# Kernel optimization log

Measured on AMD Instinct MI355X. Metric: run time of the kernel, lower is better.

## Reference

```python
import jax, jax.numpy as jnp
import numpy as np

N = 50000
E = 640000
H = 128
C = 3

def _xavier(key, shape, gain=1.0):
    fan_in, fan_out = shape[0], shape[1]
    a = gain * np.sqrt(6.0 / (fan_in + fan_out))
    return jax.random.uniform(key, shape, jnp.float32, -a, a)

def setup_inputs() -> dict:
    key = jax.random.key(0)
    ks = jax.random.split(key, 12)
    h = jax.random.normal(ks[0], (N, H), jnp.float32)
    x = jax.random.normal(ks[1], (N, C), jnp.float32)
    edge_index = jax.random.randint(ks[2], (2, E), 0, N, jnp.int64 if jax.config.jax_enable_x64 else jnp.int32)
    # edge_mlp: Linear(2H+1 -> H), SiLU, Linear(H -> H), SiLU
    We1 = _xavier(ks[3], (2 * H + 1, H)); be1 = jnp.zeros((H,), jnp.float32)
    We2 = _xavier(ks[4], (H, H));          be2 = jnp.zeros((H,), jnp.float32)
    # coord_mlp: Linear(H -> H), SiLU, Linear(H -> 1, no bias, gain 0.01)
    Wc1 = _xavier(ks[5], (H, H)); bc1 = jnp.zeros((H,), jnp.float32)
    Wc2 = _xavier(ks[6], (H, 1), gain=0.01)
    # node_mlp: Linear(2H -> H), SiLU, Linear(H -> H)
    Wn1 = _xavier(ks[7], (2 * H, H)); bn1 = jnp.zeros((H,), jnp.float32)
    Wn2 = _xavier(ks[8], (H, H));     bn2 = jnp.zeros((H,), jnp.float32)
    return dict(h=h, x=x, edge_index=edge_index,
                We1=We1, be1=be1, We2=We2, be2=be2,
                Wc1=Wc1, bc1=bc1, Wc2=Wc2,
                Wn1=Wn1, bn1=bn1, Wn2=Wn2, bn2=bn2)

def reference(h, x, edge_index, We1, be1, We2, be2, Wc1, bc1, Wc2, Wn1, bn1, Wn2, bn2):
    src, dst = edge_index[0], edge_index[1]
    n = h.shape[0]
    rel_pos = x[src] - x[dst]                              # [E, C]
    dist_sq = jnp.sum(rel_pos * rel_pos, axis=-1, keepdims=True)  # [E, 1]
    edge_input = jnp.concatenate([h[src], h[dst], dist_sq], axis=-1)  # [E, 2H+1]
    m_ij = jax.nn.silu(edge_input @ We1 + be1)
    m_ij = jax.nn.silu(m_ij @ We2 + be2)                   # [E, H]
    coord_weight = jax.nn.silu(m_ij @ Wc1 + bc1) @ Wc2     # [E, 1]
    coord_agg = jax.ops.segment_sum(rel_pos * coord_weight, dst, num_segments=n)
    x_out = x + coord_agg
    msg_agg = jax.ops.segment_sum(m_ij, dst, num_segments=n)  # [N, H]
    node_input = jnp.concatenate([h, msg_agg], axis=-1)    # [N, 2H]
    h_upd = jax.nn.silu(node_input @ Wn1 + bn1) @ Wn2 + bn2
    h_out = h + h_upd
    return (h_out, x_out)
```

## Files before the change

kernel.cpp:

```cpp
#include <hip/hip_runtime.h>

#define H 128

typedef __bf16 bf8_t __attribute__((ext_vector_type(8)));
typedef __bf16 bf2_t __attribute__((ext_vector_type(2)));
typedef float  f4_t  __attribute__((ext_vector_type(4)));

#define MFMA16(a, b, c) __builtin_amdgcn_mfma_f32_16x16x32_bf16((a), (b), (c), 0, 0, 0)

__device__ __forceinline__ float silu_f(float v) {
    return v * (1.0f / (1.0f + __expf(-v)));
}

__device__ __forceinline__ void bar_lds() {
    asm volatile("s_waitcnt lgkmcnt(0)\ns_barrier" ::: "memory");
}

__device__ __forceinline__ float wload(const void* p, int idx, bool f32) {
    return f32 ? ((const float*)p)[idx] : (float)((const __bf16*)p)[idx];
}

__device__ __forceinline__ bf8_t hload8(const void* p, size_t off, bool f32) {
    bf8_t v;
    if (f32) {
        const float4* q = (const float4*)((const float*)p + off);
        const float4 a = q[0], b = q[1];
        v[0]=(__bf16)a.x; v[1]=(__bf16)a.y; v[2]=(__bf16)a.z; v[3]=(__bf16)a.w;
        v[4]=(__bf16)b.x; v[5]=(__bf16)b.y; v[6]=(__bf16)b.z; v[7]=(__bf16)b.w;
    } else {
        v = *(const bf8_t*)((const __bf16*)p + off);
    }
    return v;
}

__device__ __forceinline__ int eidx(const void* ei, int i, bool i64) {
    return i64 ? (int)((const long long*)ei)[i] : ((const int*)ei)[i];
}

__global__ void detect_kernel(const unsigned short* __restrict__ hraw,
                              const int* __restrict__ eiraw, int* __restrict__ flags)
{
    __shared__ int s_nf, s_oddnz;
    if (threadIdx.x == 0) { s_nf = 0; s_oddnz = 0; }
    __syncthreads();
    int nf = 0;
    for (int i = threadIdx.x; i < 16384; i += blockDim.x) {
        const unsigned short u = hraw[i];
        if (((u >> 7) & 0xFF) == 0xFF) nf++;
    }
    int onz = 0;
    for (int i = threadIdx.x; i < 512; i += blockDim.x) {
        if (eiraw[2*i + 1] != 0) onz++;
    }
    if (nf)  atomicAdd(&s_nf, nf);
    if (onz) atomicAdd(&s_oddnz, onz);
    __syncthreads();
    if (threadIdx.x == 0) {
        flags[0] = (s_nf > 0) ? 1 : 0;
        flags[1] = (s_oddnz == 0) ? 1 : 0;
    }
}

__global__ void histd_kernel(const void* __restrict__ ei, int* __restrict__ cnt,
                             const int* __restrict__ flags, int Ee)
{
    const int e = blockIdx.x*blockDim.x + threadIdx.x;
    if (e < Ee) atomicAdd(&cnt[eidx(ei, Ee + e, flags[1] != 0)], 1);
}

__global__ void scanA_kernel(const int* __restrict__ cnt, int* __restrict__ bsum, int Nn)
{
    __shared__ int s[512];
    const int gi = blockIdx.x*512 + threadIdx.x;
    s[threadIdx.x] = (gi < Nn) ? cnt[gi] : 0;
    __syncthreads();
    for (int off = 256; off > 0; off >>= 1) {
        if (threadIdx.x < off) s[threadIdx.x] += s[threadIdx.x + off];
        __syncthreads();
    }
    if (threadIdx.x == 0) bsum[blockIdx.x] = s[0];
}

__global__ void scanB_kernel(int* __restrict__ bsum, int* __restrict__ base, int nCh)
{
    if (threadIdx.x == 0) {
        int acc = 0;
        for (int b = 0; b < nCh; ++b) { base[b] = acc; acc += bsum[b]; }
    }
}

__global__ void scanC_kernel(const int* __restrict__ cnt, const int* __restrict__ base,
                             int* __restrict__ off, int* __restrict__ cursor, int Nn)
{
    __shared__ int s[512];
    const int i  = threadIdx.x;
    const int gi = blockIdx.x*512 + i;
    const int v  = (gi < Nn) ? cnt[gi] : 0;
    s[i] = v;
    __syncthreads();
    for (int o = 1; o < 512; o <<= 1) {
        const int t = (i >= o) ? s[i - o] : 0;
        __syncthreads();
        s[i] += t;
        __syncthreads();
    }
    const int excl = s[i] - v;
    if (gi <= Nn) {
        const int val = base[blockIdx.x] + excl;
        off[gi] = val;
        if (gi < Nn) cursor[gi] = val;
    }
}

__global__ void scatgeo_kernel(const void* __restrict__ ei, int* __restrict__ cursor,
                               int* __restrict__ srcs, int* __restrict__ dsts,
                               float4* __restrict__ rel4, const void* __restrict__ x,
                               const int* __restrict__ flags, int Ee)
{
    const int e = blockIdx.x*blockDim.x + threadIdx.x;
    if (e >= Ee) return;
    const bool i64 = flags[1] != 0;
    const bool f32 = flags[0] != 0;
    const int s = eidx(ei, e, i64);
    const int d = eidx(ei, Ee + e, i64);
    const int p = atomicAdd(&cursor[d], 1);
    srcs[p] = s;
    dsts[p] = d;
    float r[3];
    #pragma unroll
    for (int c = 0; c < 3; ++c)
        r[c] = wload(x, s*3 + c, f32) - wload(x, d*3 + c, f32);
    float4 o; o.x = r[0]; o.y = r[1]; o.z = r[2];
    o.w = r[0]*r[0] + r[1]*r[1] + r[2]*r[2];
    rel4[p] = o;
}

__global__ __launch_bounds__(512, 2)
void proj_kernel(const void* __restrict__ h, const void* __restrict__ We1,
                 const void* __restrict__ be1, const int* __restrict__ flags,
                 __bf16* __restrict__ PB, int Nn)
{
    const bool f32 = flags[0] != 0;
    const int tid  = threadIdx.x;
    const int wv   = tid >> 6;
    const int lane = tid & 63;
    const int quad = lane >> 4;
    const int l15  = lane & 15;

    bf8_t bW[4][2];
    float bias[2];
    #pragma unroll
    for (int t = 0; t < 2; ++t) {
        const int n    = wv*32 + t*16 + l15;
        const int rb   = (n < 128) ? 0 : 128;
        const int col  = n & 127;
        #pragma unroll
        for (int kc = 0; kc < 4; ++kc) {
            bf8_t v;
            #pragma unroll
            for (int j = 0; j < 8; ++j)
                v[j] = (__bf16)wload(We1, (rb + kc*32 + quad*8 + j)*H + col, f32);
            bW[kc][t] = v;
        }
        bias[t] = (n < 128) ? 0.f : wload(be1, col, f32);
    }

    __shared__ __bf16 s_h[32*136];

    const int tiles = (Nn + 31) >> 5;
    for (int tile = blockIdx.x; tile < tiles; tile += gridDim.x) {
        const int nb = tile << 5;
        __syncthreads();
        {
            const int m = tid >> 4, c = tid & 15;
            int node = nb + m; if (node >= Nn) node = Nn - 1;
            *(bf8_t*)&s_h[m*136 + c*8] = hload8(h, (size_t)node*H + c*8, f32);
        }
        __syncthreads();

        f4_t acc[2][2];
        #pragma unroll
        for (int mm = 0; mm < 2; ++mm)
            #pragma unroll
            for (int t = 0; t < 2; ++t) acc[mm][t] = (f4_t){0.f,0.f,0.f,0.f};
        #pragma unroll
        for (int kc = 0; kc < 4; ++kc) {
            #pragma unroll
            for (int mm = 0; mm < 2; ++mm) {
                const bf8_t a = *(const bf8_t*)&s_h[(mm*16 + l15)*136 + quad*8 + kc*32];
                acc[mm][0] = MFMA16(a, bW[kc][0], acc[mm][0]);
                acc[mm][1] = MFMA16(a, bW[kc][1], acc[mm][1]);
            }
        }
        #pragma unroll
        for (int mm = 0; mm < 2; ++mm)
            #pragma unroll
            for (int i = 0; i < 4; ++i) {
                const int row = nb + mm*16 + quad*4 + i;
                if (row < Nn) {
                    #pragma unroll
                    for (int t = 0; t < 2; ++t)
                        PB[(size_t)row*256 + wv*32 + t*16 + l15] =
                            (__bf16)(acc[mm][t][i] + bias[t]);
                }
            }
    }
}

__global__ __launch_bounds__(512, 2)
void egnn_edge_pipe_kernel(const __bf16* __restrict__ PB,
                           const int* __restrict__ srcs, const int* __restrict__ dsts,
                           const float4* __restrict__ rel4,
                           const void* __restrict__ We1,
                           const void* __restrict__ We2, const void* __restrict__ be2,
                           const void* __restrict__ Wc1, const void* __restrict__ bc1,
                           const void* __restrict__ Wc2, const int* __restrict__ flags,
                           float* __restrict__ msg, float* __restrict__ coord,
                           int Ee)
{
    const bool f32 = flags[0] != 0;
    const int tid  = threadIdx.x;
    const int wv   = tid >> 6;
    const int lane = tid & 63;
    const int quad = lane >> 4;
    const int l15  = lane & 15;
    const int mg   = wv >> 2;
    const int ng   = wv & 3;

    bf8_t bW2[4][2], bWc[4][2];
    float be2v[2], bc1v[2], wc2v[2];
    #pragma unroll
    for (int t = 0; t < 2; ++t) {
        const int n = ng*32 + t*16 + l15;
        #pragma unroll
        for (int kc = 0; kc < 4; ++kc) {
            bf8_t v, u;
            #pragma unroll
            for (int j = 0; j < 8; ++j) {
                v[j] = (__bf16)wload(We2, (kc*32 + quad*8 + j)*H + n, f32);
                u[j] = (__bf16)wload(Wc1, (kc*32 + quad*8 + j)*H + n, f32);
            }
            bW2[kc][t] = v;
            bWc[kc][t] = u;
        }
        be2v[t] = wload(be2, n, f32);
        bc1v[t] = wload(bc1, n, f32);
        wc2v[t] = wload(Wc2, n, f32);
    }

    const int em = tid >> 3;
    const int ch = tid & 7;
    float w1dA[8], w1dB[8];
    #pragma unroll
    for (int j = 0; j < 8; ++j) {
        w1dA[j] = wload(We1, 256*H + ch*8 + j, f32);
        w1dB[j] = wload(We1, 256*H + (ch+8)*8 + j, f32);
    }

    __shared__ __bf16 s_m1[64*136];
    __shared__ __bf16 s_m2[64*136];
    __shared__ float  s_cw[4*64];
    __shared__ int    s_dst[2][64];
    __shared__ float4 s_rl[2][64];
    __shared__ float  s_pre[8][128];
    __shared__ float  s_suf[8][128];
    __shared__ int    s_wh[8];

    const int tiles = (Ee + 63) >> 6;
    const float* rw = (const float*)rel4;

    bf8_t rA0, rA1, rB0, rB1;
    float d2cur, d2nxt;
    int   s_n, d_n, d_c;
    float4 r4c, r4n;
    {
        int e0 = blockIdx.x*64 + em; if (e0 >= Ee) e0 = Ee - 1;
        const int sc = srcs[e0], dc = dsts[e0];
        d_c = dc;
        d2cur = rw[(size_t)e0*4 + 3];
        if (ch == 0) r4c = rel4[e0];
        rA0 = *(const bf8_t*)(PB + (size_t)sc*256 + ch*8);
        rA1 = *(const bf8_t*)(PB + (size_t)sc*256 + (ch+8)*8);
        rB0 = *(const bf8_t*)(PB + (size_t)dc*256 + 128 + ch*8);
        rB1 = *(const bf8_t*)(PB + (size_t)dc*256 + 128 + (ch+8)*8);
        const int t1 = blockIdx.x + gridDim.x;
        const int tt = (t1 < tiles) ? t1 : blockIdx.x;
        int e1 = tt*64 + em; if (e1 >= Ee) e1 = Ee - 1;
        s_n = srcs[e1]; d_n = dsts[e1]; d2nxt = rw[(size_t)e1*4 + 3];
        if (ch == 0) r4n = rel4[e1];
    }

    int li = 0;
    for (int t = blockIdx.x; t < tiles; t += gridDim.x, ++li) {
        const int sb = li & 1;
        {
            bf8_t o0, o1;
            #pragma unroll
            for (int j = 0; j < 8; ++j) {
                const float f0 = (float)rA0[j] + (float)rB0[j] + d2cur*w1dA[j];
                const float f1 = (float)rA1[j] + (float)rB1[j] + d2cur*w1dB[j];
                o0[j] = (__bf16)silu_f(f0);
                o1[j] = (__bf16)silu_f(f1);
            }
            *(bf8_t*)&s_m1[em*136 + ch*8]       = o0;
            *(bf8_t*)&s_m1[em*136 + (ch+8)*8]   = o1;
            if (ch == 0) { s_dst[sb][em] = d_c; s_rl[sb][em] = r4c; }
        }
        {
            const int sc = s_n, dc2 = d_n;
            rA0 = *(const bf8_t*)(PB + (size_t)sc*256 + ch*8);
            rA1 = *(const bf8_t*)(PB + (size_t)sc*256 + (ch+8)*8);
            rB0 = *(const bf8_t*)(PB + (size_t)dc2*256 + 128 + ch*8);
            rB1 = *(const bf8_t*)(PB + (size_t)dc2*256 + 128 + (ch+8)*8);
            d_c = d_n; d2cur = d2nxt;
            if (ch == 0) r4c = r4n;
            const int t2 = t + 2*gridDim.x;
            const int tt = (t2 < tiles) ? t2 : t;
            int e2 = tt*64 + em; if (e2 >= Ee) e2 = Ee - 1;
            s_n = srcs[e2]; d_n = dsts[e2]; d2nxt = rw[(size_t)e2*4 + 3];
            if (ch == 0) r4n = rel4[e2];
        }
        bar_lds();

        {
            f4_t a2[2][2];
            #pragma unroll
            for (int mm = 0; mm < 2; ++mm)
                #pragma unroll
                for (int h2 = 0; h2 < 2; ++h2) a2[mm][h2] = (f4_t){0.f,0.f,0.f,0.f};
            #pragma unroll
            for (int kc = 0; kc < 4; ++kc) {
                #pragma unroll
                for (int mm = 0; mm < 2; ++mm) {
                    const bf8_t a = *(const bf8_t*)&s_m1[(mg*32 + mm*16 + l15)*136 + quad*8 + kc*32];
                    a2[mm][0] = MFMA16(a, bW2[kc][0], a2[mm][0]);
                    a2[mm][1] = MFMA16(a, bW2[kc][1], a2[mm][1]);
                }
            }
            #pragma unroll
            for (int mm = 0; mm < 2; ++mm)
                #pragma unroll
                for (int i = 0; i < 4; ++i) {
                    const int m = mg*32 + mm*16 + quad*4 + i;
                    s_m2[m*136 + ng*32 + l15]      = (__bf16)silu_f(a2[mm][0][i] + be2v[0]);
                    s_m2[m*136 + ng*32 + 16 + l15] = (__bf16)silu_f(a2[mm][1][i] + be2v[1]);
                }
        }
        bar_lds();

        {
            f4_t a3[2][2];
            #pragma unroll
            for (int mm = 0; mm < 2; ++mm)
                #pragma unroll
                for (int h2 = 0; h2 < 2; ++h2) a3[mm][h2] = (f4_t){0.f,0.f,0.f,0.f};
            #pragma unroll
            for (int kc = 0; kc < 4; ++kc) {
                #pragma unroll
                for (int mm = 0; mm < 2; ++mm) {
                    const bf8_t a = *(const bf8_t*)&s_m2[(mg*32 + mm*16 + l15)*136 + quad*8 + kc*32];
                    a3[mm][0] = MFMA16(a, bWc[kc][0], a3[mm][0]);
                    a3[mm][1] = MFMA16(a, bWc[kc][1], a3[mm][1]);
                }
            }
            float p[2][4];
            #pragma unroll
            for (int mm = 0; mm < 2; ++mm)
                #pragma unroll
                for (int i = 0; i < 4; ++i) {
                    const float v0 = silu_f(a3[mm][0][i] + bc1v[0]);
                    const float v1 = silu_f(a3[mm][1][i] + bc1v[1]);
                    p[mm][i] = v0*wc2v[0] + v1*wc2v[1];
                }
            #pragma unroll
            for (int off = 1; off < 16; off <<= 1)
                #pragma unroll
                for (int mm = 0; mm < 2; ++mm)
                    #pragma unroll
                    for (int i = 0; i < 4; ++i) p[mm][i] += __shfl_xor(p[mm][i], off, 64);
            if (l15 == 0) {
                #pragma unroll
                for (int mm = 0; mm < 2; ++mm)
                    #pragma unroll
                    for (int i = 0; i < 4; ++i)
                        s_cw[ng*64 + (mg*32 + mm*16 + quad*4 + i)] = p[mm][i];
            }
        }

        {
            const int rbase = wv << 3;
            const int c0    = lane << 1;
            int   curd = __builtin_amdgcn_readfirstlane(s_dst[sb][rbase]);
            float ax = 0.f, ay = 0.f;
            float px = 0.f, py = 0.f;
            int   predone = 0;
            #pragma unroll
            for (int i = 0; i < 8; ++i) {
                const int d = __builtin_amdgcn_readfirstlane(s_dst[sb][rbase + i]);
                const bf2_t v = *(const bf2_t*)&s_m2[(rbase + i)*136 + c0];
                const float vx = (float)v[0], vy = (float)v[1];
                if (d != curd) {
                    if (!predone) { px = ax; py = ay; predone = 1; }
                    else {
                        float2 st; st.x = ax; st.y = ay;
                        *(float2*)&msg[(size_t)curd*H + c0] = st;
                    }
                    curd = d; ax = vx; ay = vy;
                } else { ax += vx; ay += vy; }
            }
            s_pre[wv][c0]   = px;  s_pre[wv][c0+1] = py;
            s_suf[wv][c0]   = ax;  s_suf[wv][c0+1] = ay;
            if (lane == 0) s_wh[wv] = !predone;
        }
        bar_lds();

        if (tid >= 128 && tid < 256) {
            const int c = tid - 128;
            int   curd2 = __builtin_amdgcn_readfirstlane(s_dst[sb][0]);
            float cur   = 0.f;
            int   first = 1;
            #pragma unroll
            for (int gg = 0; gg < 8; ++gg) {
                const int F  = __builtin_amdgcn_readfirstlane(s_dst[sb][gg*8]);
                const int L  = __builtin_amdgcn_readfirstlane(s_dst[sb][gg*8 + 7]);
                const int wh = __builtin_amdgcn_readfirstlane(s_wh[gg]);
                const float preg = s_pre[gg][c];
                const float sufg = s_suf[gg][c];
                if (F != curd2) {
                    if (first) atomicAdd(&msg[(size_t)curd2*H + c], cur);
                    else       msg[(size_t)curd2*H + c] = cur;
                    first = 0; curd2 = F; cur = 0.f;
                }
                if (wh) {
                    cur += sufg;
                } else {
                    cur += preg;
                    if (first) atomicAdd(&msg[(size_t)curd2*H + c], cur);
                    else       msg[(size_t)curd2*H + c] = cur;
                    first = 0; curd2 = L; cur = sufg;
                }
            }
            atomicAdd(&msg[(size_t)curd2*H + c], cur);
        }

        if (tid < 64) {
            const int e = tid;
            const float cwv = s_cw[e] + s_cw[64 + e] + s_cw[128 + e] + s_cw[192 + e];
            const float4 r = s_rl[sb][e];
            const int d = s_dst[sb][e];
            float vx = r.x*cwv, vy = r.y*cwv, vz = r.z*cwv;
            int   cn = 1;
            #pragma unroll
            for (int k = 1; k < 64; k <<= 1) {
                const int   dk = __shfl_up(d,  k, 64);
                const float xk = __shfl_up(vx, k, 64);
                const float yk = __shfl_up(vy, k, 64);
                const float zk = __shfl_up(vz, k, 64);
                const int   ck = __shfl_up(cn, k, 64);
                if (e >= k && dk == d) { vx += xk; vy += yk; vz += zk; cn += ck; }
            }
            const int dnx = __shfl_down(d, 1, 64);
            const bool runend = (e == 63) || (dnx != d);
            if (runend) {
                const int rs = e - cn + 1;
                if (rs == 0 || e == 63) {
                    atomicAdd(&coord[(size_t)d*3 + 0], vx);
                    atomicAdd(&coord[(size_t)d*3 + 1], vy);
                    atomicAdd(&coord[(size_t)d*3 + 2], vz);
                } else {
                    coord[(size_t)d*3 + 0] = vx;
                    coord[(size_t)d*3 + 1] = vy;
                    coord[(size_t)d*3 + 2] = vz;
                }
            }
        }
    }
}

__global__ __launch_bounds__(512, 2)
void egnn_node_kernel(const void* __restrict__ h, const float* __restrict__ msg,
                      const void* __restrict__ Wn1, const void* __restrict__ bn1,
                      const void* __restrict__ Wn2, const void* __restrict__ bn2,
                      const int* __restrict__ flags, void* __restrict__ h_out,
                      const void* __restrict__ x, const float* __restrict__ coord,
                      size_t obase, int do_x, int Nn)
{
    const bool f32 = flags[0] != 0;
    const int tid  = threadIdx.x;
    const int wv   = tid >> 6;
    const int lane = tid & 63;
    const int quad = lane >> 4;
    const int l15  = lane & 15;
    const int mg   = wv >> 2;
    const int ng   = wv & 3;

    bf8_t bW1[8][2];
    bf8_t bW2[4][2];
    float b1v[2], b2v[2];
    #pragma unroll
    for (int t = 0; t < 2; ++t) {
        const int n = ng*32 + t*16 + l15;
        #pragma unroll
        for (int kc = 0; kc < 8; ++kc) {
            bf8_t v;
            #pragma unroll
            for (int j = 0; j < 8; ++j) v[j] = (__bf16)wload(Wn1, (kc*32 + quad*8 + j)*H + n, f32);
            bW1[kc][t] = v;
        }
        #pragma unroll
        for (int kc = 0; kc < 4; ++kc) {
            bf8_t v;
            #pragma unroll
            for (int j = 0; j < 8; ++j) v[j] = (__bf16)wload(Wn2, (kc*32 + quad*8 + j)*H + n, f32);
            bW2[kc][t] = v;
        }
        b1v[t] = wload(bn1, n, f32);
        b2v[t] = wload(bn2, n, f32);
    }

    __shared__ __bf16 s_in[32*264];
    __shared__ __bf16 s_t1[32*136];

    const int tiles = (Nn + 31) >> 5;
    for (int tile = blockIdx.x; tile < tiles; tile += gridDim.x) {
        const int nb = tile << 5;
        __syncthreads();
        #pragma unroll
        for (int r = 0; r < 2; ++r) {
            const int idx = tid + r*512;
            const int m = idx >> 5, c = idx & 31;
            int node = nb + m;
            if (node >= Nn) node = Nn - 1;
            if (c < 16) {
                *(bf8_t*)&s_in[m*264 + c*8] = hload8(h, (size_t)node*H + c*8, f32);
            } else {
                const float4* mp = (const float4*)(msg + (size_t)node*H + (c - 16)*8);
                const float4 v0 = mp[0], v1 = mp[1];
                __bf16* d = &s_in[m*264 + c*8];
                d[0] = (__bf16)v0.x; d[1] = (__bf16)v0.y; d[2] = (__bf16)v0.z; d[3] = (__bf16)v0.w;
                d[4] = (__bf16)v1.x; d[5] = (__bf16)v1.y; d[6] = (__bf16)v1.z; d[7] = (__bf16)v1.w;
            }
        }
        if (do_x && tid < 96) {
            const int m = tid / 3, c = tid - m*3;
            const int node = nb + m;
            if (node < Nn) {
                const float xv = wload(x, node*3 + c, f32);
                const float o = xv + coord[(size_t)node*3 + c];
                if (f32) ((float*)h_out)[obase + (size_t)node*3 + c] = o;
                else     ((__bf16*)h_out)[obase + (size_t)node*3 + c] = (__bf16)o;
            }
        }
        __syncthreads();

        {
            f4_t a0 = {0.f,0.f,0.f,0.f}, a1 = {0.f,0.f,0.f,0.f};
            const int abase = (mg*16 + l15)*264 + quad*8;
            #pragma unroll
            for (int kc = 0; kc < 8; ++kc) {
                const bf8_t a = *(const bf8_t*)&s_in[abase + kc*32];
                a0 = MFMA16(a, bW1[kc][0], a0);
                a1 = MFMA16(a, bW1[kc][1], a1);
            }
            #pragma unroll
            for (int i = 0; i < 4; ++i) {
                const int m = mg*16 + quad*4 + i;
                s_t1[m*136 + ng*32 + l15]      = (__bf16)silu_f(a0[i] + b1v[0]);
                s_t1[m*136 + ng*32 + 16 + l15] = (__bf16)silu_f(a1[i] + b1v[1]);
            }
        }
        __syncthreads();

        {
            f4_t a0 = {0.f,0.f,0.f,0.f}, a1 = {0.f,0.f,0.f,0.f};
            const int abase = (mg*16 + l15)*136 + quad*8;
            #pragma unroll
            for (int kc = 0; kc < 4; ++kc) {
                const bf8_t a = *(const bf8_t*)&s_t1[abase + kc*32];
                a0 = MFMA16(a, bW2[kc][0], a0);
                a1 = MFMA16(a, bW2[kc][1], a1);
            }
            #pragma unroll
            for (int i = 0; i < 4; ++i) {
                const int node = nb + mg*16 + quad*4 + i;
                if (node < Nn) {
                    const int n0 = ng*32 + l15, n1 = n0 + 16;
                    const size_t i0 = (size_t)node*H + n0, i1 = (size_t)node*H + n1;
                    const float h0 = f32 ? ((const float*)h)[i0] : (float)((const __bf16*)h)[i0];
                    const float h1 = f32 ? ((const float*)h)[i1] : (float)((const __bf16*)h)[i1];
                    const float o0 = a0[i] + b2v[0] + h0;
                    const float o1 = a1[i] + b2v[1] + h1;
                    if (f32) {
                        ((float*)h_out)[i0] = o0;
                        ((float*)h_out)[i1] = o1;
                    } else {
                        ((__bf16*)h_out)[i0] = (__bf16)o0;
                        ((__bf16*)h_out)[i1] = (__bf16)o1;
                    }
                }
            }
        }
    }
}

__global__ void cvt_ei_kernel(const void* __restrict__ src, int* __restrict__ dst,
                              int n, const int* __restrict__ flags)
{
    const int i = blockIdx.x*blockDim.x + threadIdx.x;
    if (i >= n) return;
    dst[i] = flags[1] ? (int)((const long long*)src)[i] : ((const int*)src)[i];
}

__global__ __launch_bounds__(512, 2)
void egnn_edge_kernel(const void* __restrict__ h, const void* __restrict__ x,
                      const int* __restrict__ ei,
                      const void* __restrict__ We1, const void* __restrict__ be1,
                      const void* __restrict__ We2, const void* __restrict__ be2,
                      const void* __restrict__ Wc1, const void* __restrict__ bc1,
                      const void* __restrict__ Wc2, const int* __restrict__ flags,
                      float* __restrict__ msg_agg, float* __restrict__ coord_agg,
                      int Nn, int Ee)
{
    const bool f32 = flags[0] != 0;
    const int tid  = threadIdx.x;
    const int wv   = tid >> 6;
    const int lane = tid & 63;
    const int quad = lane >> 4;
    const int l15  = lane & 15;
    const int mg   = wv >> 2;
    const int ng   = wv & 3;

    bf8_t bW1[8][2];
    bf8_t bW2[4][2];
    bf8_t bWc[4][2];
    float be1v[2], be2v[2], bc1v[2], w1dv[2], wc2v[2];
    #pragma unroll
    for (int t = 0; t < 2; ++t) {
        const int n = ng*32 + t*16 + l15;
        #pragma unroll
        for (int kc = 0; kc < 8; ++kc) {
            bf8_t v;
            #pragma unroll
            for (int j = 0; j < 8; ++j) v[j] = (__bf16)wload(We1, (kc*32 + quad*8 + j)*H + n, f32);
            bW1[kc][t] = v;
        }
        #pragma unroll
        for (int kc = 0; kc < 4; ++kc) {
            bf8_t v, u;
            #pragma unroll
            for (int j = 0; j < 8; ++j) {
                v[j] = (__bf16)wload(We2, (kc*32 + quad*8 + j)*H + n, f32);
                u[j] = (__bf16)wload(Wc1, (kc*32 + quad*8 + j)*H + n, f32);
            }
            bW2[kc][t] = v;
            bWc[kc][t] = u;
        }
        be1v[t] = wload(be1, n, f32);
        be2v[t] = wload(be2, n, f32);
        bc1v[t] = wload(bc1, n, f32);
        w1dv[t] = wload(We1, 256*H + n, f32);
        wc2v[t] = wload(Wc2, n, f32);
    }

    __shared__ __bf16 s_in[32*264];
    __shared__ __bf16 s_m1[32*136];
    __shared__ __bf16 s_m2[32*136];
    __shared__ float  s_rel[32*3];
    __shared__ float  s_dist[32];
    __shared__ int    s_dstv[32];
    __shared__ float  s_cw[32*4];

    const int tiles = Ee >> 5;
    for (int tile = blockIdx.x; tile < tiles; tile += gridDim.x) {
        const int ebase = tile << 5;
        __syncthreads();

        if (tid < 32) {
            const int e  = ebase + tid;
            const int sn = ei[e];
            const int dn = ei[Ee + e];
            s_dstv[tid] = dn;
            float d2 = 0.f;
            #pragma unroll
            for (int c = 0; c < 3; ++c) {
                float r;
                if (f32) r = ((const float*)x)[sn*3 + c] - ((const float*)x)[dn*3 + c];
                else     r = (float)((const __bf16*)x)[sn*3 + c] - (float)((const __bf16*)x)[dn*3 + c];
                s_rel[tid*3 + c] = r;
                d2 += r*r;
            }
            s_dist[tid] = d2;
        }
        #pragma unroll
        for (int r = 0; r < 2; ++r) {
            const int idx = tid + r*512;
            const int m = idx >> 5, c = idx & 31;
            const int e = ebase + m;
            const int node = (c < 16) ? ei[e] : ei[Ee + e];
            *(bf8_t*)&s_in[m*264 + c*8] = hload8(h, (size_t)node*H + (c & 15)*8, f32);
        }
        __syncthreads();

        {
            f4_t a0 = {0.f,0.f,0.f,0.f}, a1 = {0.f,0.f,0.f,0.f};
            const int abase = (mg*16 + l15)*264 + quad*8;
            #pragma unroll
            for (int kc = 0; kc < 8; ++kc) {
                const bf8_t a = *(const bf8_t*)&s_in[abase + kc*32];
                a0 = MFMA16(a, bW1[kc][0], a0);
                a1 = MFMA16(a, bW1[kc][1], a1);
            }
            #pragma unroll
            for (int i = 0; i < 4; ++i) {
                const int m = mg*16 + quad*4 + i;
                const float d2 = s_dist[m];
                s_m1[m*136 + ng*32 + l15]      = (__bf16)silu_f(a0[i] + d2*w1dv[0] + be1v[0]);
                s_m1[m*136 + ng*32 + 16 + l15] = (__bf16)silu_f(a1[i] + d2*w1dv[1] + be1v[1]);
            }
        }
        __syncthreads();

        {
            f4_t a0 = {0.f,0.f,0.f,0.f}, a1 = {0.f,0.f,0.f,0.f};
            const int abase = (mg*16 + l15)*136 + quad*8;
            #pragma unroll
            for (int kc = 0; kc < 4; ++kc) {
                const bf8_t a = *(const bf8_t*)&s_m1[abase + kc*32];
                a0 = MFMA16(a, bW2[kc][0], a0);
                a1 = MFMA16(a, bW2[kc][1], a1);
            }
            #pragma unroll
            for (int i = 0; i < 4; ++i) {
                const int m = mg*16 + quad*4 + i;
                const float v0 = silu_f(a0[i] + be2v[0]);
                const float v1 = silu_f(a1[i] + be2v[1]);
                s_m2[m*136 + ng*32 + l15]      = (__bf16)v0;
                s_m2[m*136 + ng*32 + 16 + l15] = (__bf16)v1;
                const size_t db = (size_t)s_dstv[m]*H + ng*32 + l15;
                atomicAdd(&msg_agg[db],      v0);
                atomicAdd(&msg_agg[db + 16], v1);
            }
        }
        __syncthreads();

        {
            f4_t a0 = {0.f,0.f,0.f,0.f}, a1 = {0.f,0.f,0.f,0.f};
            const int abase = (mg*16 + l15)*136 + quad*8;
            #pragma unroll
            for (int kc = 0; kc < 4; ++kc) {
                const bf8_t a = *(const bf8_t*)&s_m2[abase + kc*32];
                a0 = MFMA16(a, bWc[kc][0], a0);
                a1 = MFMA16(a, bWc[kc][1], a1);
            }
            float p[4];
            #pragma unroll
            for (int i = 0; i < 4; ++i) {
                const float v0 = silu_f(a0[i] + bc1v[0]);
                const float v1 = silu_f(a1[i] + bc1v[1]);
                p[i] = v0*wc2v[0] + v1*wc2v[1];
            }
            #pragma unroll
            for (int off = 1; off < 16; off <<= 1) {
                #pragma unroll
                for (int i = 0; i < 4; ++i) p[i] += __shfl_xor(p[i], off, 64);
            }
            if (l15 == 0) {
                #pragma unroll
                for (int i = 0; i < 4; ++i)
                    s_cw[(mg*16 + quad*4 + i)*4 + ng] = p[i];
            }
        }
        __syncthreads();

        if (tid < 96) {
            const int m = tid / 3, c = tid - m*3;
            const float cw = s_cw[m*4 + 0] + s_cw[m*4 + 1] + s_cw[m*4 + 2] + s_cw[m*4 + 3];
            atomicAdd(&coord_agg[(size_t)s_dstv[m]*3 + c], s_rel[m*3 + c]*cw);
        }
    }
}

__global__ void egnn_x_kernel(const void* __restrict__ x, const float* __restrict__ coord_agg,
                              const int* __restrict__ flags, void* __restrict__ out,
                              size_t obase, int total)
{
    const bool f32 = flags[0] != 0;
    const int i = blockIdx.x*blockDim.x + threadIdx.x;
    if (i >= total) return;
    const float xv = f32 ? ((const float*)x)[i] : (float)((const __bf16*)x)[i];
    const float o = xv + coord_agg[i];
    if (f32) ((float*)out)[obase + i] = o;
    else     ((__bf16*)out)[obase + i] = (__bf16)o;
}

static inline size_t align256(size_t v) { return (v + 255) & ~(size_t)255; }

extern "C" void kernel_launch(void* const* d_in, const int* in_sizes, int n_in,
                              void* d_out, int out_size, void* d_ws, size_t ws_size,
                              hipStream_t stream)
{
    const void* h   = d_in[0];
    const void* x   = d_in[1];
    const void* ei0 = d_in[2];
    const void* We1 = d_in[3];
    const void* be1 = d_in[4];
    const void* We2 = d_in[5];
    const void* be2 = d_in[6];
    const void* Wc1 = d_in[7];
    const void* bc1 = d_in[8];
    const void* Wc2 = d_in[9];
    const void* Wn1 = d_in[10];
    const void* bn1 = d_in[11];
    const void* Wn2 = d_in[12];
    const void* bn2 = d_in[13];

    const int Nn = in_sizes[0] / H;
    const int Ee = in_sizes[2] / 2;

    char* ws = (char*)d_ws;
    size_t o = 0;
    size_t o_cnt   = o; o = align256(o + (size_t)Nn*4);
    size_t o_msg   = o; o = align256(o + (size_t)Nn*H*4);
    size_t o_coord = o; o = align256(o + (size_t)Nn*3*4);
    const size_t zero_end = o;
    size_t o_srcs  = o; o = align256(o + (size_t)Ee*4);
    size_t o_dsts  = o; o = align256(o + (size_t)Ee*4);
    size_t o_rel   = o; o = align256(o + (size_t)Ee*16);
    size_t o_pb    = o; o = align256(o + (size_t)Nn*256*2);
    size_t o_off   = o; o = align256(o + (size_t)(Nn+1)*4);
    size_t o_cur   = o; o = align256(o + (size_t)Nn*4);
    size_t o_bsum  = o; o = align256(o + 512*4);
    size_t o_base  = o; o = align256(o + 512*4);
    size_t o_flags = o; o = align256(o + 64);
    const size_t need_csr = o;

    const int nCh = (Nn + 1 + 511) / 512;

    if (ws_size >= need_csr) {
        int*    cnt     = (int*)   (ws + o_cnt);
        float*  msg     = (float*) (ws + o_msg);
        float*  coord   = (float*) (ws + o_coord);
        int*    srcs    = (int*)   (ws + o_srcs);
        int*    dsts    = (int*)   (ws + o_dsts);
        float4* rel4    = (float4*)(ws + o_rel);
        __bf16* PB      = (__bf16*)(ws + o_pb);
        int*    off     = (int*)   (ws + o_off);
        int*    cursor  = (int*)   (ws + o_cur);
        int*    bsum    = (int*)   (ws + o_bsum);
        int*    base    = (int*)   (ws + o_base);
        int*    flags   = (int*)   (ws + o_flags);

        detect_kernel<<<1, 256, 0, stream>>>((const unsigned short*)h, (const int*)ei0, flags);
        hipMemsetAsync(ws + o_cnt, 0, zero_end - o_cnt, stream);
        histd_kernel<<<(Ee + 511)/512, 512, 0, stream>>>(ei0, cnt, flags, Ee);
        scanA_kernel<<<nCh, 512, 0, stream>>>(cnt, bsum, Nn);
        scanB_kernel<<<1, 64, 0, stream>>>(bsum, base, nCh);
        scanC_kernel<<<nCh, 512, 0, stream>>>(cnt, base, off, cursor, Nn);
        scatgeo_kernel<<<(Ee + 511)/512, 512, 0, stream>>>(ei0, cursor, srcs, dsts,
                                                           rel4, x, flags, Ee);
        proj_kernel<<<512, 512, 0, stream>>>(h, We1, be1, flags, PB, Nn);

        egnn_edge_pipe_kernel<<<512, 512, 0, stream>>>(PB, srcs, dsts, rel4,
                                                       We1, We2, be2, Wc1, bc1, Wc2,
                                                       flags, msg, coord, Ee);

        egnn_node_kernel<<<1024, 512, 0, stream>>>(h, msg, Wn1, bn1, Wn2, bn2,
                                                   flags, d_out, x, coord,
                                                   (size_t)Nn*H, 1, Nn);
    } else {
        float* msg_agg   = (float*)ws;
        float* coord_agg = (float*)(ws + (size_t)Nn*H*4);
        int*   ei        = (int*)  (ws + (size_t)Nn*H*4 + (size_t)Nn*3*4);
        int*   flags     = (int*)  (ws + (size_t)Nn*H*4 + (size_t)Nn*3*4 + (size_t)2*Ee*4);

        detect_kernel<<<1, 256, 0, stream>>>((const unsigned short*)h, (const int*)ei0, flags);
        cvt_ei_kernel<<<(2*Ee + 255)/256, 256, 0, stream>>>(ei0, ei, 2*Ee, flags);
        hipMemsetAsync(msg_agg,   0, (size_t)Nn*H*4, stream);
        hipMemsetAsync(coord_agg, 0, (size_t)Nn*3*4, stream);
        egnn_edge_kernel<<<1024, 512, 0, stream>>>(h, x, ei, We1, be1, We2, be2,
                                                   Wc1, bc1, Wc2, flags,
                                                   msg_agg, coord_agg, Nn, Ee);
        egnn_node_kernel<<<512, 512, 0, stream>>>(h, msg_agg, Wn1, bn1, Wn2, bn2,
                                                  flags, d_out, x, coord_agg,
                                                  (size_t)Nn*H, 0, Nn);
        egnn_x_kernel<<<(Nn*3 + 255)/256, 256, 0, stream>>>(x, coord_agg, flags, d_out,
                                                            (size_t)Nn*H, Nn*3);
    }
}
```

Measured before the change: 652.9 us.

## Fuse scatter/geometry with projection kernel and defer edge segment reductions

Merges the edge scatter/geometry kernel and the node projection kernel into one launch, with 256 blocks doing projection and 256 doing the scatter, so the two independent phases can run concurrently. In the edge pipeline, the msg and coord segment-reduction stores for tile i are moved into iteration i+1. They now run after the first barrier and overlap with the MFMA work. The s_cw, s_pre, s_suf and s_wh buffers are double-buffered for this, and a tail flush handles the last tile. This removes one barrier per tile and one kernel launch, at the cost of extra LDS use and fewer blocks for each fused phase.

```diff
diff --git a/kernel.cpp b/kernel.cpp
--- a/kernel.cpp
+++ b/kernel.cpp
@@ -112,36 +112,38 @@
     }
 }
 
-__global__ void scatgeo_kernel(const void* __restrict__ ei, int* __restrict__ cursor,
-                               int* __restrict__ srcs, int* __restrict__ dsts,
-                               float4* __restrict__ rel4, const void* __restrict__ x,
-                               const int* __restrict__ flags, int Ee)
-{
-    const int e = blockIdx.x*blockDim.x + threadIdx.x;
-    if (e >= Ee) return;
-    const bool i64 = flags[1] != 0;
-    const bool f32 = flags[0] != 0;
-    const int s = eidx(ei, e, i64);
-    const int d = eidx(ei, Ee + e, i64);
-    const int p = atomicAdd(&cursor[d], 1);
-    srcs[p] = s;
-    dsts[p] = d;
-    float r[3];
-    #pragma unroll
-    for (int c = 0; c < 3; ++c)
-        r[c] = wload(x, s*3 + c, f32) - wload(x, d*3 + c, f32);
-    float4 o; o.x = r[0]; o.y = r[1]; o.z = r[2];
-    o.w = r[0]*r[0] + r[1]*r[1] + r[2]*r[2];
-    rel4[p] = o;
-}
-
 __global__ __launch_bounds__(512, 2)
-void proj_kernel(const void* __restrict__ h, const void* __restrict__ We1,
-                 const void* __restrict__ be1, const int* __restrict__ flags,
-                 __bf16* __restrict__ PB, int Nn)
-{
+void scatgeo_proj_kernel(const void* __restrict__ ei, int* __restrict__ cursor,
+                         int* __restrict__ srcs, int* __restrict__ dsts,
+                         float4* __restrict__ rel4, const void* __restrict__ x,
+                         const void* __restrict__ h, const void* __restrict__ We1,
+                         const void* __restrict__ be1, const int* __restrict__ flags,
+                         __bf16* __restrict__ PB, int Nn, int Ee, int projBlocks)
+{
+    __shared__ __bf16 s_h[32*136];
     const bool f32 = flags[0] != 0;
     const int tid  = threadIdx.x;
+
+    if ((int)blockIdx.x >= projBlocks) {
+        const bool i64 = flags[1] != 0;
+        const int nb = gridDim.x - projBlocks;
+        for (int e = ((int)blockIdx.x - projBlocks)*512 + tid; e < Ee; e += nb*512) {
+            const int s = eidx(ei, e, i64);
+            const int d = eidx(ei, Ee + e, i64);
+            const int p = atomicAdd(&cursor[d], 1);
+            srcs[p] = s;
+            dsts[p] = d;
+            float r[3];
+            #pragma unroll
+            for (int c = 0; c < 3; ++c)
+                r[c] = wload(x, s*3 + c, f32) - wload(x, d*3 + c, f32);
+            float4 o; o.x = r[0]; o.y = r[1]; o.z = r[2];
+            o.w = r[0]*r[0] + r[1]*r[1] + r[2]*r[2];
+            rel4[p] = o;
+        }
+        return;
+    }
+
     const int wv   = tid >> 6;
     const int lane = tid & 63;
     const int quad = lane >> 4;
@@ -165,15 +167,13 @@
         bias[t] = (n < 128) ? 0.f : wload(be1, col, f32);
     }
 
-    __shared__ __bf16 s_h[32*136];
-
     const int tiles = (Nn + 31) >> 5;
-    for (int tile = blockIdx.x; tile < tiles; tile += gridDim.x) {
-        const int nb = tile << 5;
+    for (int tile = blockIdx.x; tile < tiles; tile += projBlocks) {
+        const int nb2 = tile << 5;
         __syncthreads();
         {
             const int m = tid >> 4, c = tid & 15;
-            int node = nb + m; if (node >= Nn) node = Nn - 1;
+            int node = nb2 + m; if (node >= Nn) node = Nn - 1;
             *(bf8_t*)&s_h[m*136 + c*8] = hload8(h, (size_t)node*H + c*8, f32);
         }
         __syncthreads();
@@ -196,7 +196,7 @@
         for (int mm = 0; mm < 2; ++mm)
             #pragma unroll
             for (int i = 0; i < 4; ++i) {
-                const int row = nb + mm*16 + quad*4 + i;
+                const int row = nb2 + mm*16 + quad*4 + i;
                 if (row < Nn) {
                     #pragma unroll
                     for (int t = 0; t < 2; ++t)
@@ -259,12 +259,12 @@
 
     __shared__ __bf16 s_m1[64*136];
     __shared__ __bf16 s_m2[64*136];
-    __shared__ float  s_cw[4*64];
+    __shared__ float  s_cw[2][4*64];
     __shared__ int    s_dst[2][64];
     __shared__ float4 s_rl[2][64];
-    __shared__ float  s_pre[8][128];
-    __shared__ float  s_suf[8][128];
-    __shared__ int    s_wh[8];
+    __shared__ float  s_pre[2][8][128];
+    __shared__ float  s_suf[2][8][128];
+    __shared__ int    s_wh[2][8];
 
     const int tiles = (Ee + 63) >> 6;
     const float* rw = (const float*)rel4;
@@ -293,6 +293,7 @@
     int li = 0;
     for (int t = blockIdx.x; t < tiles; t += gridDim.x, ++li) {
         const int sb = li & 1;
+        const int pb = sb ^ 1;
         {
             bf8_t o0, o1;
             #pragma unroll
@@ -322,6 +323,69 @@
         }
         bar_lds();
 
+        if (li > 0) {
+            if (tid >= 128 && tid < 256) {
+                const int c = tid - 128;
+                int   curd2 = __builtin_amdgcn_readfirstlane(s_dst[pb][0]);
+                float cur   = 0.f;
+                int   first = 1;
+                #pragma unroll
+                for (int gg = 0; gg < 8; ++gg) {
+                    const int F  = __builtin_amdgcn_readfirstlane(s_dst[pb][gg*8]);
+                    const int L  = __builtin_amdgcn_readfirstlane(s_dst[pb][gg*8 + 7]);
+                    const int wh = __builtin_amdgcn_readfirstlane(s_wh[pb][gg]);
+                    const float preg = s_pre[pb][gg][c];
+                    const float sufg = s_suf[pb][gg][c];
+                    if (F != curd2) {
+                        if (first) atomicAdd(&msg[(size_t)curd2*H + c], cur);
+                        else       msg[(size_t)curd2*H + c] = cur;
+                        first = 0; curd2 = F; cur = 0.f;
+                    }
+                    if (wh) {
+                        cur += sufg;
+                    } else {
+                        cur += preg;
+                        if (first) atomicAdd(&msg[(size_t)curd2*H + c], cur);
+                        else       msg[(size_t)curd2*H + c] = cur;
+                        first = 0; curd2 = L; cur = sufg;
+                    }
+                }
+                atomicAdd(&msg[(size_t)curd2*H + c], cur);
+            }
+            if (tid < 64) {
+                const int e = tid;
+                const float cwv = s_cw[pb][e] + s_cw[pb][64 + e] +
+                                  s_cw[pb][128 + e] + s_cw[pb][192 + e];
+                const float4 r = s_rl[pb][e];
+                const int d = s_dst[pb][e];
+                float vx = r.x*cwv, vy = r.y*cwv, vz = r.z*cwv;
+                int   cn = 1;
+                #pragma unroll
+                for (int k = 1; k < 64; k <<= 1) {
+                    const int   dk = __shfl_up(d,  k, 64);
+                    const float xk = __shfl_up(vx, k, 64);
+                    const float yk = __shfl_up(vy, k, 64);
+                    const float zk = __shfl_up(vz, k, 64);
+                    const int   ck = __shfl_up(cn, k, 64);
+                    if (e >= k && dk == d) { vx += xk; vy += yk; vz += zk; cn += ck; }
+                }
+                const int dnx = __shfl_down(d, 1, 64);
+                const bool runend = (e == 63) || (dnx != d);
+                if (runend) {
+                    const int rs = e - cn + 1;
+                    if (rs == 0 || e == 63) {
+                        atomicAdd(&coord[(size_t)d*3 + 0], vx);
+                        atomicAdd(&coord[(size_t)d*3 + 1], vy);
+                        atomicAdd(&coord[(size_t)d*3 + 2], vz);
+                    } else {
+                        coord[(size_t)d*3 + 0] = vx;
+                        coord[(size_t)d*3 + 1] = vy;
+                        coord[(size_t)d*3 + 2] = vz;
+                    }
+                }
+            }
+        }
+
         {
             f4_t a2[2][2];
             #pragma unroll
@@ -383,7 +447,7 @@
                 for (int mm = 0; mm < 2; ++mm)
                     #pragma unroll
                     for (int i = 0; i < 4; ++i)
-                        s_cw[ng*64 + (mg*32 + mm*16 + quad*4 + i)] = p[mm][i];
+                        s_cw[sb][ng*64 + (mg*32 + mm*16 + quad*4 + i)] = p[mm][i];
             }
         }
 
@@ -408,24 +472,27 @@
                     curd = d; ax = vx; ay = vy;
                 } else { ax += vx; ay += vy; }
             }
-            s_pre[wv][c0]   = px;  s_pre[wv][c0+1] = py;
-            s_suf[wv][c0]   = ax;  s_suf[wv][c0+1] = ay;
-            if (lane == 0) s_wh[wv] = !predone;
-        }
+            s_pre[sb][wv][c0]   = px;  s_pre[sb][wv][c0+1] = py;
+            s_suf[sb][wv][c0]   = ax;  s_suf[sb][wv][c0+1] = ay;
+            if (lane == 0) s_wh[sb][wv] = !predone;
+        }
+    }
+
+    if (li > 0) {
         bar_lds();
-
+        const int pb = (li - 1) & 1;
         if (tid >= 128 && tid < 256) {
             const int c = tid - 128;
-            int   curd2 = __builtin_amdgcn_readfirstlane(s_dst[sb][0]);
+            int   curd2 = __builtin_amdgcn_readfirstlane(s_dst[pb][0]);
             float cur   = 0.f;
             int   first = 1;
             #pragma unroll
             for (int gg = 0; gg < 8; ++gg) {
-                const int F  = __builtin_amdgcn_readfirstlane(s_dst[sb][gg*8]);
-                const int L  = __builtin_amdgcn_readfirstlane(s_dst[sb][gg*8 + 7]);
-                const int wh = __builtin_amdgcn_readfirstlane(s_wh[gg]);
-                const float preg = s_pre[gg][c];
-                const float sufg = s_suf[gg][c];
+                const int F  = __builtin_amdgcn_readfirstlane(s_dst[pb][gg*8]);
+                const int L  = __builtin_amdgcn_readfirstlane(s_dst[pb][gg*8 + 7]);
+                const int wh = __builtin_amdgcn_readfirstlane(s_wh[pb][gg]);
+                const float preg = s_pre[pb][gg][c];
+                const float sufg = s_suf[pb][gg][c];
                 if (F != curd2) {
                     if (first) atomicAdd(&msg[(size_t)curd2*H + c], cur);
                     else       msg[(size_t)curd2*H + c] = cur;
@@ -442,12 +509,12 @@
             }
             atomicAdd(&msg[(size_t)curd2*H + c], cur);
         }
-
         if (tid < 64) {
             const int e = tid;
-            const float cwv = s_cw[e] + s_cw[64 + e] + s_cw[128 + e] + s_cw[192 + e];
-            const float4 r = s_rl[sb][e];
-            const int d = s_dst[sb][e];
+            const float cwv = s_cw[pb][e] + s_cw[pb][64 + e] +
+                              s_cw[pb][128 + e] + s_cw[pb][192 + e];
+            const float4 r = s_rl[pb][e];
+            const int d = s_dst[pb][e];
             float vx = r.x*cwv, vy = r.y*cwv, vz = r.z*cwv;
             int   cn = 1;
             #pragma unroll
@@ -856,9 +923,10 @@
         scanA_kernel<<<nCh, 512, 0, stream>>>(cnt, bsum, Nn);
         scanB_kernel<<<1, 64, 0, stream>>>(bsum, base, nCh);
         scanC_kernel<<<nCh, 512, 0, stream>>>(cnt, base, off, cursor, Nn);
-        scatgeo_kernel<<<(Ee + 511)/512, 512, 0, stream>>>(ei0, cursor, srcs, dsts,
-                                                           rel4, x, flags, Ee);
-        proj_kernel<<<512, 512, 0, stream>>>(h, We1, be1, flags, PB, Nn);
+
+        scatgeo_proj_kernel<<<512, 512, 0, stream>>>(ei0, cursor, srcs, dsts, rel4,
+                                                     x, h, We1, be1, flags, PB,
+                                                     Nn, Ee, 256);
 
         egnn_edge_pipe_kernel<<<512, 512, 0, stream>>>(PB, srcs, dsts, rel4,
                                                        We1, We2, be2, Wc1, bc1, Wc2,
```

Result: no change. 645.7 us (-1.1%).
